# Kernel optimization log

Measured on AMD Instinct MI355X. Metric: run time of the kernel, lower is better.

## Reference

```python
import jax, jax.numpy as jnp
import numpy as np

N = 100000
E = 1600000
D = 64
BETA = 1.0


def setup_inputs() -> dict:
    key = jax.random.key(0)
    ks = jax.random.split(key, 6)
    x = jax.random.normal(ks[0], (N, D), dtype=jnp.float32)
    edge_index = jax.random.randint(ks[1], (2, E), 0, N, dtype=jnp.int64)
    s = 1.0 / np.sqrt(D)
    Wm = jax.random.uniform(ks[2], (D, D), jnp.float32, -s, s)
    bm = jax.random.uniform(ks[3], (D,), jnp.float32, -s, s)
    Wr = jax.random.uniform(ks[4], (D, D), jnp.float32, -s, s)
    br = jax.random.uniform(ks[5], (D,), jnp.float32, -s, s)
    return {"x": x, "edge_index": edge_index, "Wm": Wm, "bm": bm, "Wr": Wr, "br": br}


def reference(x, edge_index, Wm, bm, Wr, br):
    row, col = edge_index[0], edge_index[1]
    # gather source features and apply message linear: [E, D]
    messages = x[row] @ Wm + bm
    scores = BETA * messages.mean(axis=-1)  # [E]
    # edge softmax over incoming edges of each destination node (col)
    seg_max = jax.ops.segment_max(scores, col, num_segments=N)  # [N]
    ex = jnp.exp(scores - seg_max[col])  # [E]
    seg_sum = jax.ops.segment_sum(ex, col, num_segments=N)  # [N]
    weights = ex / seg_sum[col]  # [E]
    # weighted scatter-add back to destinations
    out = jax.ops.segment_sum(messages * weights[:, None], col, num_segments=N)
    return out + (x @ Wr + br)
```

## Files before the change

kernel.cpp:

```cpp
#include <hip/hip_runtime.h>
#include <math.h>

#define N_NODES 100000
#define DIM 64
#define N_EDGES 1600000

#define NBF 1563
#define BK_NODES 64
#define CAP 1408

#define SC_CHUNK 8192
#define SC_BLOCKS ((N_EDGES + SC_CHUNK - 1) / SC_CHUNK)

#define GEMM_BLOCKS ((N_NODES / 16 + 15) / 16)
#define PH_BLOCKS (SC_BLOCKS + GEMM_BLOCKS)

typedef _Float16 half8 __attribute__((ext_vector_type(8)));
typedef _Float16 half4 __attribute__((ext_vector_type(4)));
typedef float f32x4 __attribute__((ext_vector_type(4)));

__global__ __launch_bounds__(1024) void k_prep(
        const float* __restrict__ Wm, const float* __restrict__ Wr,
        _Float16* __restrict__ Wt, int* __restrict__ cursor) {
    const int t = threadIdx.x;
    for (int i = t; i < NBF; i += 1024) cursor[i] = 0;
#pragma unroll
    for (int k = 0; k < 8; ++k) {
        const int i = k * 1024 + t;
        const int c = i >> 6;
        const int kk = i & 63;
        const float v = (c < 64) ? Wm[kk * 64 + c] : Wr[kk * 64 + (c - 64)];
        Wt[i] = (_Float16)v;
    }
}

__global__ __launch_bounds__(1024) void k_phase(
        const float* __restrict__ x,
        const _Float16* __restrict__ Wt,
        const float* __restrict__ bm, const float* __restrict__ br,
        const int* __restrict__ row, const int* __restrict__ col,
        int* __restrict__ cursor, unsigned int* __restrict__ pairs,
        _Float16* __restrict__ Mh, float* __restrict__ es,
        float* __restrict__ out) {
    __shared__ int cnt[NBF];
    __shared__ int basg[NBF];

    const int t = threadIdx.x;
    const int lane = t & 63;
    const int wid = t >> 6;

    if (blockIdx.x < SC_BLOCKS) {
        const int start = blockIdx.x * SC_CHUNK;
        const int mEnd = min(N_EDGES, start + SC_CHUNK);

        for (int i = t; i < NBF; i += 1024) cnt[i] = 0;
        __syncthreads();

        int rr[8], cc[8], lr[8];
#pragma unroll
        for (int k = 0; k < 8; ++k) {
            const int idx = start + k * 1024 + t;
            if (idx < mEnd) {
                cc[k] = col[idx];
                rr[k] = row[idx];
                lr[k] = atomicAdd(&cnt[cc[k] >> 6], 1);
            }
        }
        __syncthreads();

        for (int i = t; i < NBF; i += 1024) {
            const int v = cnt[i];
            if (v > 0) basg[i] = atomicAdd(&cursor[i], v);
        }
        __syncthreads();

#pragma unroll
        for (int k = 0; k < 8; ++k) {
            const int idx = start + k * 1024 + t;
            if (idx < mEnd) {
                const int bk = cc[k] >> 6;
                const int gslot = basg[bk] + lr[k];
                if (gslot < CAP)
                    pairs[(size_t)bk * CAP + gslot] =
                        ((unsigned int)rr[k] << 6) | (unsigned int)(cc[k] & 63);
            }
        }
        return;
    }

    const int wave = (blockIdx.x - SC_BLOCKS) * 16 + wid;
    if (wave >= N_NODES / 16) return;
    const int quad = lane >> 4;
    const int l15 = lane & 15;
    const int row0 = wave * 16;

    const half8* __restrict__ Wt8 = (const half8*)Wt;
    half8 bfrag[8][2];
#pragma unroll
    for (int ct = 0; ct < 8; ++ct) {
        const int cidx = ((ct < 4) ? 0 : 64) + (ct & 3) * 16 + l15;
#pragma unroll
        for (int kc = 0; kc < 2; ++kc)
            bfrag[ct][kc] = Wt8[cidx * 8 + kc * 4 + quad];
    }

    half8 afrag[2];
#pragma unroll
    for (int kc = 0; kc < 2; ++kc) {
        const float* xp = x + (size_t)(row0 + l15) * DIM + kc * 32 + quad * 8;
        const float4 x0 = *(const float4*)xp;
        const float4 x1 = *(const float4*)(xp + 4);
        half8 f;
        f[0] = (_Float16)x0.x; f[1] = (_Float16)x0.y;
        f[2] = (_Float16)x0.z; f[3] = (_Float16)x0.w;
        f[4] = (_Float16)x1.x; f[5] = (_Float16)x1.y;
        f[6] = (_Float16)x1.z; f[7] = (_Float16)x1.w;
        afrag[kc] = f;
    }

    f32x4 acc[8];
#pragma unroll
    for (int ct = 0; ct < 8; ++ct) {
        f32x4 a = {0.f, 0.f, 0.f, 0.f};
        a = __builtin_amdgcn_mfma_f32_16x16x32_f16(afrag[0], bfrag[ct][0], a, 0, 0, 0);
        a = __builtin_amdgcn_mfma_f32_16x16x32_f16(afrag[1], bfrag[ct][1], a, 0, 0, 0);
        acc[ct] = a;
    }

    float rsum[4] = {0.f, 0.f, 0.f, 0.f};
#pragma unroll
    for (int ct = 0; ct < 8; ++ct) {
        const float bias = (ct < 4) ? bm[(ct & 3) * 16 + l15]
                                    : br[(ct & 3) * 16 + l15];
#pragma unroll
        for (int r = 0; r < 4; ++r) {
            const float v = acc[ct][r] + bias;
            const size_t idx = (size_t)(row0 + quad * 4 + r) * DIM + (ct & 3) * 16 + l15;
            if (ct < 4) {
                Mh[idx] = (_Float16)v;
                rsum[r] += v;
            } else {
                out[idx] = v;
            }
        }
    }
#pragma unroll
    for (int o = 1; o <= 8; o <<= 1) {
#pragma unroll
        for (int r = 0; r < 4; ++r) rsum[r] += __shfl_xor(rsum[r], o, 64);
    }
    if (l15 == 0) {
#pragma unroll
        for (int r = 0; r < 4; ++r)
            es[row0 + quad * 4 + r] = __expf(rsum[r] * (1.0f / DIM));
    }
}

__global__ __launch_bounds__(512) void k_bucket_gather(
        const unsigned int* __restrict__ pairs, const int* __restrict__ cursor,
        const float* __restrict__ es, const half4* __restrict__ Mh4,
        float4* __restrict__ out4) {
    __shared__ unsigned int sorted[CAP];
    __shared__ int cnt[BK_NODES];
    __shared__ int off[BK_NODES];
    const int b = blockIdx.x;
    const int t = threadIdx.x;
    const int lane = t & 63;
    const int wid = t >> 6;
    const int m = min(cursor[b], CAP);
    const size_t base = (size_t)b * CAP;

    if (t < BK_NODES) cnt[t] = 0;
    __syncthreads();

    unsigned int pk[3];
    int rk[3];
#pragma unroll
    for (int k = 0; k < 3; ++k) {
        const int i = k * 512 + t;
        if (i < m) {
            pk[k] = pairs[base + i];
            rk[k] = atomicAdd(&cnt[pk[k] & 63u], 1);
        }
    }
    __syncthreads();

    if (wid == 0) {
        const int v = cnt[lane];
        int inc = v;
#pragma unroll
        for (int o = 1; o < 64; o <<= 1) {
            const int u = __shfl_up(inc, o, 64);
            if (lane >= o) inc += u;
        }
        off[lane] = inc - v;
    }
    __syncthreads();

#pragma unroll
    for (int k = 0; k < 3; ++k) {
        const int i = k * 512 + t;
        if (i < m) sorted[off[pk[k] & 63u] + rk[k]] = pk[k];
    }
    __syncthreads();

    const int g = t >> 4;
    const int gl = t & 15;
    for (int c = g; c < BK_NODES; c += 32) {
        const int node = b * BK_NODES + c;
        if (node >= N_NODES) break;
        const int s0i = off[c];
        const int len = cnt[c];
        if (len == 0) continue;

        float a0x = 0.f, a0y = 0.f, a0z = 0.f, a0w = 0.f, l0 = 0.f;
        float a1x = 0.f, a1y = 0.f, a1z = 0.f, a1w = 0.f, l1 = 0.f;
        float a2x = 0.f, a2y = 0.f, a2z = 0.f, a2w = 0.f, l2 = 0.f;
        float a3x = 0.f, a3y = 0.f, a3z = 0.f, a3w = 0.f, l3 = 0.f;
        int j = 0;
        for (; j + 3 < len; j += 4) {
            const int s0 = (int)(sorted[s0i + j] >> 6);
            const int s1 = (int)(sorted[s0i + j + 1] >> 6);
            const int s2 = (int)(sorted[s0i + j + 2] >> 6);
            const int s3 = (int)(sorted[s0i + j + 3] >> 6);
            const float w0 = es[s0];
            const float w1 = es[s1];
            const float w2 = es[s2];
            const float w3 = es[s3];
            const half4 m0 = Mh4[(size_t)s0 * 16 + gl];
            const half4 m1 = Mh4[(size_t)s1 * 16 + gl];
            const half4 m2 = Mh4[(size_t)s2 * 16 + gl];
            const half4 m3 = Mh4[(size_t)s3 * 16 + gl];
            l0 += w0; l1 += w1; l2 += w2; l3 += w3;
            a0x = fmaf(w0, (float)m0[0], a0x); a0y = fmaf(w0, (float)m0[1], a0y);
            a0z = fmaf(w0, (float)m0[2], a0z); a0w = fmaf(w0, (float)m0[3], a0w);
            a1x = fmaf(w1, (float)m1[0], a1x); a1y = fmaf(w1, (float)m1[1], a1y);
            a1z = fmaf(w1, (float)m1[2], a1z); a1w = fmaf(w1, (float)m1[3], a1w);
            a2x = fmaf(w2, (float)m2[0], a2x); a2y = fmaf(w2, (float)m2[1], a2y);
            a2z = fmaf(w2, (float)m2[2], a2z); a2w = fmaf(w2, (float)m2[3], a2w);
            a3x = fmaf(w3, (float)m3[0], a3x); a3y = fmaf(w3, (float)m3[1], a3y);
            a3z = fmaf(w3, (float)m3[2], a3z); a3w = fmaf(w3, (float)m3[3], a3w);
        }
        for (; j < len; ++j) {
            const int s0 = (int)(sorted[s0i + j] >> 6);
            const float w0 = es[s0];
            const half4 m0 = Mh4[(size_t)s0 * 16 + gl];
            l0 += w0;
            a0x = fmaf(w0, (float)m0[0], a0x); a0y = fmaf(w0, (float)m0[1], a0y);
            a0z = fmaf(w0, (float)m0[2], a0z); a0w = fmaf(w0, (float)m0[3], a0w);
        }
        const float inv = 1.0f / (l0 + l1 + l2 + l3);
        float4 r = out4[(size_t)node * 16 + gl];
        r.x = fmaf(a0x + a1x + a2x + a3x, inv, r.x);
        r.y = fmaf(a0y + a1y + a2y + a3y, inv, r.y);
        r.z = fmaf(a0z + a1z + a2z + a3z, inv, r.z);
        r.w = fmaf(a0w + a1w + a2w + a3w, inv, r.w);
        out4[(size_t)node * 16 + gl] = r;
    }
}

extern "C" void kernel_launch(void* const* d_in, const int* in_sizes, int n_in,
                              void* d_out, int out_size, void* d_ws, size_t ws_size,
                              hipStream_t stream) {
    const float* x  = (const float*)d_in[0];
    const int*   ei = (const int*)d_in[1];
    const float* Wm = (const float*)d_in[2];
    const float* bm = (const float*)d_in[3];
    const float* Wr = (const float*)d_in[4];
    const float* br = (const float*)d_in[5];
    float* out = (float*)d_out;
    const int* row = ei;
    const int* col = ei + N_EDGES;

    char* ws = (char*)d_ws;
    _Float16* Mh    = (_Float16*)ws;     ws += (size_t)N_NODES * DIM * sizeof(_Float16);
    float* es       = (float*)ws;        ws += (size_t)N_NODES * sizeof(float);
    int* cursor     = (int*)ws;          ws += (size_t)2048 * sizeof(int);
    _Float16* Wt    = (_Float16*)ws;     ws += (size_t)128 * 64 * sizeof(_Float16);
    unsigned int* pairs = (unsigned int*)ws; ws += (size_t)NBF * CAP * sizeof(unsigned int);

    k_prep<<<1, 1024, 0, stream>>>(Wm, Wr, Wt, cursor);
    k_phase<<<PH_BLOCKS, 1024, 0, stream>>>(x, Wt, bm, br, row, col,
                                            cursor, pairs, Mh, es, out);
    k_bucket_gather<<<NBF, 512, 0, stream>>>(pairs, cursor, es,
                                             (const half4*)Mh, (float4*)out);
}
```

Baseline: 167.1 us.

## Split fused scatter/GEMM phase kernel into separate scatter and GEMM kernels

The merged phase kernel, which ran edge bucketing and the node GEMM in different blocks of one 1024-thread launch, is split into a 512-thread scatter kernel (smaller edge chunks, a single reused shared count array) and a 256-thread GEMM kernel. The prep kernel now uses many blocks to zero the cursors, and its weight transpose reads the weights with coalesced loads. The aim is better occupancy and less shared memory per block for each phase, since the fused kernel forced both halves onto the GEMM's 1024-thread shape. The cost is an extra launch and the loss of overlap between scatter and GEMM inside a single grid.

```diff
diff --git a/kernel.cpp b/kernel.cpp
--- a/kernel.cpp
+++ b/kernel.cpp
@@ -9,11 +9,10 @@
 #define BK_NODES 64
 #define CAP 1408
 
-#define SC_CHUNK 8192
+#define SC_CHUNK 4096
 #define SC_BLOCKS ((N_EDGES + SC_CHUNK - 1) / SC_CHUNK)
 
-#define GEMM_BLOCKS ((N_NODES / 16 + 15) / 16)
-#define PH_BLOCKS (SC_BLOCKS + GEMM_BLOCKS)
+#define GEMM_BLOCKS ((N_NODES / 16 + 3) / 4)
 
 typedef _Float16 half8 __attribute__((ext_vector_type(8)));
 typedef _Float16 half4 __attribute__((ext_vector_type(4)));
@@ -22,73 +21,73 @@
 __global__ __launch_bounds__(1024) void k_prep(
         const float* __restrict__ Wm, const float* __restrict__ Wr,
         _Float16* __restrict__ Wt, int* __restrict__ cursor) {
+    const int gid = blockIdx.x * 1024 + threadIdx.x;
+    if (gid < NBF) cursor[gid] = 0;
+    if (blockIdx.x == gridDim.x - 1) {
+        const int t = threadIdx.x;
+#pragma unroll
+        for (int k = 0; k < 4; ++k) {
+            const int i = k * 1024 + t;
+            const int kk = i >> 6;
+            const int c = i & 63;
+            Wt[c * 64 + kk] = (_Float16)Wm[i];
+            Wt[(64 + c) * 64 + kk] = (_Float16)Wr[i];
+        }
+    }
+}
+
+__global__ __launch_bounds__(512) void k_scatter(
+        const int* __restrict__ row, const int* __restrict__ col,
+        int* __restrict__ cursor, unsigned int* __restrict__ pairs) {
+    __shared__ int cnt[NBF];
     const int t = threadIdx.x;
-    for (int i = t; i < NBF; i += 1024) cursor[i] = 0;
+    const int start = blockIdx.x * SC_CHUNK;
+    const int mEnd = min(N_EDGES, start + SC_CHUNK);
+
+    for (int i = t; i < NBF; i += 512) cnt[i] = 0;
+    __syncthreads();
+
+    int rr[8], cc[8], lr[8];
 #pragma unroll
     for (int k = 0; k < 8; ++k) {
-        const int i = k * 1024 + t;
-        const int c = i >> 6;
-        const int kk = i & 63;
-        const float v = (c < 64) ? Wm[kk * 64 + c] : Wr[kk * 64 + (c - 64)];
-        Wt[i] = (_Float16)v;
-    }
-}
-
-__global__ __launch_bounds__(1024) void k_phase(
+        const int idx = start + k * 512 + t;
+        if (idx < mEnd) {
+            cc[k] = col[idx];
+            rr[k] = row[idx];
+            lr[k] = atomicAdd(&cnt[cc[k] >> 6], 1);
+        }
+    }
+    __syncthreads();
+
+    for (int i = t; i < NBF; i += 512) {
+        const int v = cnt[i];
+        if (v > 0) cnt[i] = atomicAdd(&cursor[i], v);
+    }
+    __syncthreads();
+
+#pragma unroll
+    for (int k = 0; k < 8; ++k) {
+        const int idx = start + k * 512 + t;
+        if (idx < mEnd) {
+            const int bk = cc[k] >> 6;
+            const int gslot = cnt[bk] + lr[k];
+            if (gslot < CAP)
+                pairs[(size_t)bk * CAP + gslot] =
+                    ((unsigned int)rr[k] << 6) | (unsigned int)(cc[k] & 63);
+        }
+    }
+}
+
+__global__ __launch_bounds__(256) void k_gemm(
         const float* __restrict__ x,
         const _Float16* __restrict__ Wt,
         const float* __restrict__ bm, const float* __restrict__ br,
-        const int* __restrict__ row, const int* __restrict__ col,
-        int* __restrict__ cursor, unsigned int* __restrict__ pairs,
         _Float16* __restrict__ Mh, float* __restrict__ es,
         float* __restrict__ out) {
-    __shared__ int cnt[NBF];
-    __shared__ int basg[NBF];
-
     const int t = threadIdx.x;
     const int lane = t & 63;
     const int wid = t >> 6;
-
-    if (blockIdx.x < SC_BLOCKS) {
-        const int start = blockIdx.x * SC_CHUNK;
-        const int mEnd = min(N_EDGES, start + SC_CHUNK);
-
-        for (int i = t; i < NBF; i += 1024) cnt[i] = 0;
-        __syncthreads();
-
-        int rr[8], cc[8], lr[8];
-#pragma unroll
-        for (int k = 0; k < 8; ++k) {
-            const int idx = start + k * 1024 + t;
-            if (idx < mEnd) {
-                cc[k] = col[idx];
-                rr[k] = row[idx];
-                lr[k] = atomicAdd(&cnt[cc[k] >> 6], 1);
-            }
-        }
-        __syncthreads();
-
-        for (int i = t; i < NBF; i += 1024) {
-            const int v = cnt[i];
-            if (v > 0) basg[i] = atomicAdd(&cursor[i], v);
-        }
-        __syncthreads();
-
-#pragma unroll
-        for (int k = 0; k < 8; ++k) {
-            const int idx = start + k * 1024 + t;
-            if (idx < mEnd) {
-                const int bk = cc[k] >> 6;
-                const int gslot = basg[bk] + lr[k];
-                if (gslot < CAP)
-                    pairs[(size_t)bk * CAP + gslot] =
-                        ((unsigned int)rr[k] << 6) | (unsigned int)(cc[k] & 63);
-            }
-        }
-        return;
-    }
-
-    const int wave = (blockIdx.x - SC_BLOCKS) * 16 + wid;
+    const int wave = blockIdx.x * 4 + wid;
     if (wave >= N_NODES / 16) return;
     const int quad = lane >> 4;
     const int l15 = lane & 15;
@@ -156,7 +155,7 @@
     }
 }
 
-__global__ __launch_bounds__(512) void k_bucket_gather(
+__global__ __launch_bounds__(512) void k_gather(
         const unsigned int* __restrict__ pairs, const int* __restrict__ cursor,
         const float* __restrict__ es, const half4* __restrict__ Mh4,
         float4* __restrict__ out4) {
@@ -279,9 +278,9 @@
     _Float16* Wt    = (_Float16*)ws;     ws += (size_t)128 * 64 * sizeof(_Float16);
     unsigned int* pairs = (unsigned int*)ws; ws += (size_t)NBF * CAP * sizeof(unsigned int);
 
-    k_prep<<<1, 1024, 0, stream>>>(Wm, Wr, Wt, cursor);
-    k_phase<<<PH_BLOCKS, 1024, 0, stream>>>(x, Wt, bm, br, row, col,
-                                            cursor, pairs, Mh, es, out);
-    k_bucket_gather<<<NBF, 512, 0, stream>>>(pairs, cursor, es,
-                                             (const half4*)Mh, (float4*)out);
-}
+    k_prep<<<128, 1024, 0, stream>>>(Wm, Wr, Wt, cursor);
+    k_scatter<<<SC_BLOCKS, 512, 0, stream>>>(row, col, cursor, pairs);
+    k_gemm<<<GEMM_BLOCKS, 256, 0, stream>>>(x, Wt, bm, br, Mh, es, out);
+    k_gather<<<NBF, 512, 0, stream>>>(pairs, cursor, es,
+                                      (const half4*)Mh, (float4*)out);
+}
```

Result: slower. 174.8 us (+4.6%).

## Drop weight-prep kernel, halve block size, and reuse shared count array for bases

Applied to the files above, without the earlier changes.

Removes the single-block k_prep kernel. The cursor array is now zeroed with hipMemsetAsync, and each GEMM wave converts Wm/Wr from fp32 to fp16 directly with strided loads instead of reading a pre-transposed fp16 copy. Blocks shrink from 1024 to 512 threads, with smaller scatter chunks and fewer GEMM waves per block. The global base offsets are stored back into the shared count array, which drops the second shared array, and edge loads are issued before the count array is cleared. This saves a launch and a serial kernel. In exchange, every GEMM wave does redundant uncoalesced weight loads and conversions.

```diff
diff --git a/kernel.cpp b/kernel.cpp
--- a/kernel.cpp
+++ b/kernel.cpp
@@ -9,41 +9,26 @@
 #define BK_NODES 64
 #define CAP 1408
 
-#define SC_CHUNK 8192
+#define SC_CHUNK 4096
 #define SC_BLOCKS ((N_EDGES + SC_CHUNK - 1) / SC_CHUNK)
 
-#define GEMM_BLOCKS ((N_NODES / 16 + 15) / 16)
+#define GEMM_WAVES 8
+#define GEMM_BLOCKS ((N_NODES / 16 + GEMM_WAVES - 1) / GEMM_WAVES)
 #define PH_BLOCKS (SC_BLOCKS + GEMM_BLOCKS)
 
 typedef _Float16 half8 __attribute__((ext_vector_type(8)));
 typedef _Float16 half4 __attribute__((ext_vector_type(4)));
 typedef float f32x4 __attribute__((ext_vector_type(4)));
 
-__global__ __launch_bounds__(1024) void k_prep(
-        const float* __restrict__ Wm, const float* __restrict__ Wr,
-        _Float16* __restrict__ Wt, int* __restrict__ cursor) {
-    const int t = threadIdx.x;
-    for (int i = t; i < NBF; i += 1024) cursor[i] = 0;
-#pragma unroll
-    for (int k = 0; k < 8; ++k) {
-        const int i = k * 1024 + t;
-        const int c = i >> 6;
-        const int kk = i & 63;
-        const float v = (c < 64) ? Wm[kk * 64 + c] : Wr[kk * 64 + (c - 64)];
-        Wt[i] = (_Float16)v;
-    }
-}
-
-__global__ __launch_bounds__(1024) void k_phase(
+__global__ __launch_bounds__(512) void k_phase(
         const float* __restrict__ x,
-        const _Float16* __restrict__ Wt,
-        const float* __restrict__ bm, const float* __restrict__ br,
+        const float* __restrict__ Wm, const float* __restrict__ bm,
+        const float* __restrict__ Wr, const float* __restrict__ br,
         const int* __restrict__ row, const int* __restrict__ col,
         int* __restrict__ cursor, unsigned int* __restrict__ pairs,
         _Float16* __restrict__ Mh, float* __restrict__ es,
         float* __restrict__ out) {
     __shared__ int cnt[NBF];
-    __shared__ int basg[NBF];
 
     const int t = threadIdx.x;
     const int lane = t & 63;
@@ -53,33 +38,37 @@
         const int start = blockIdx.x * SC_CHUNK;
         const int mEnd = min(N_EDGES, start + SC_CHUNK);
 
-        for (int i = t; i < NBF; i += 1024) cnt[i] = 0;
-        __syncthreads();
-
         int rr[8], cc[8], lr[8];
 #pragma unroll
         for (int k = 0; k < 8; ++k) {
-            const int idx = start + k * 1024 + t;
+            const int idx = start + k * 512 + t;
             if (idx < mEnd) {
                 cc[k] = col[idx];
                 rr[k] = row[idx];
-                lr[k] = atomicAdd(&cnt[cc[k] >> 6], 1);
             }
         }
+        for (int i = t; i < NBF; i += 512) cnt[i] = 0;
         __syncthreads();
 
-        for (int i = t; i < NBF; i += 1024) {
+#pragma unroll
+        for (int k = 0; k < 8; ++k) {
+            const int idx = start + k * 512 + t;
+            if (idx < mEnd) lr[k] = atomicAdd(&cnt[cc[k] >> 6], 1);
+        }
+        __syncthreads();
+
+        for (int i = t; i < NBF; i += 512) {
             const int v = cnt[i];
-            if (v > 0) basg[i] = atomicAdd(&cursor[i], v);
+            if (v > 0) cnt[i] = atomicAdd(&cursor[i], v);
         }
         __syncthreads();
 
 #pragma unroll
         for (int k = 0; k < 8; ++k) {
-            const int idx = start + k * 1024 + t;
+            const int idx = start + k * 512 + t;
             if (idx < mEnd) {
                 const int bk = cc[k] >> 6;
-                const int gslot = basg[bk] + lr[k];
+                const int gslot = cnt[bk] + lr[k];
                 if (gslot < CAP)
                     pairs[(size_t)bk * CAP + gslot] =
                         ((unsigned int)rr[k] << 6) | (unsigned int)(cc[k] & 63);
@@ -88,20 +77,25 @@
         return;
     }
 
-    const int wave = (blockIdx.x - SC_BLOCKS) * 16 + wid;
+    const int wave = (blockIdx.x - SC_BLOCKS) * GEMM_WAVES + wid;
     if (wave >= N_NODES / 16) return;
     const int quad = lane >> 4;
     const int l15 = lane & 15;
     const int row0 = wave * 16;
 
-    const half8* __restrict__ Wt8 = (const half8*)Wt;
     half8 bfrag[8][2];
 #pragma unroll
     for (int ct = 0; ct < 8; ++ct) {
-        const int cidx = ((ct < 4) ? 0 : 64) + (ct & 3) * 16 + l15;
-#pragma unroll
-        for (int kc = 0; kc < 2; ++kc)
-            bfrag[ct][kc] = Wt8[cidx * 8 + kc * 4 + quad];
+        const float* W = (ct < 4) ? Wm : Wr;
+        const int c = (ct & 3) * 16 + l15;
+#pragma unroll
+        for (int kc = 0; kc < 2; ++kc) {
+            half8 f;
+#pragma unroll
+            for (int j = 0; j < 8; ++j)
+                f[j] = (_Float16)W[(kc * 32 + quad * 8 + j) * DIM + c];
+            bfrag[ct][kc] = f;
+        }
     }
 
     half8 afrag[2];
@@ -276,12 +270,12 @@
     _Float16* Mh    = (_Float16*)ws;     ws += (size_t)N_NODES * DIM * sizeof(_Float16);
     float* es       = (float*)ws;        ws += (size_t)N_NODES * sizeof(float);
     int* cursor     = (int*)ws;          ws += (size_t)2048 * sizeof(int);
-    _Float16* Wt    = (_Float16*)ws;     ws += (size_t)128 * 64 * sizeof(_Float16);
     unsigned int* pairs = (unsigned int*)ws; ws += (size_t)NBF * CAP * sizeof(unsigned int);
 
-    k_prep<<<1, 1024, 0, stream>>>(Wm, Wr, Wt, cursor);
-    k_phase<<<PH_BLOCKS, 1024, 0, stream>>>(x, Wt, bm, br, row, col,
-                                            cursor, pairs, Mh, es, out);
+    hipMemsetAsync(cursor, 0, NBF * sizeof(int), stream);
+
+    k_phase<<<PH_BLOCKS, 512, 0, stream>>>(x, Wm, bm, Wr, br, row, col,
+                                           cursor, pairs, Mh, es, out);
     k_bucket_gather<<<NBF, 512, 0, stream>>>(pairs, cursor, es,
                                              (const half4*)Mh, (float4*)out);
 }
```

Result: no change. 165.2 us (-1.1%).
